# Kernel optimization log

Hardware: AMD Instinct MI355X
Metric: run time of the kernel (lower is better)

## Reference

```python
import jax, jax.numpy as jnp
import numpy as np

O, T, DIN, H, DOUT = 50000, 500000, 128, 256, 128


def setup_inputs() -> dict:
    key = jax.random.key(0)
    ks = jax.random.split(key, 12)
    s = 0.05
    return {
        "obj_vecs": jax.random.normal(ks[0], (O, DIN), jnp.float32),
        "pred_vecs": jax.random.normal(ks[1], (T, DIN), jnp.float32),
        "edges": jax.random.randint(ks[2], (T, 2), 0, O, jnp.int64),
        "w1a": jax.random.normal(ks[3], (3 * DIN, H), jnp.float32) * s,
        "b1a": jax.random.normal(ks[4], (H,), jnp.float32) * s,
        "w1b": jax.random.normal(ks[5], (H, 2 * H + DOUT), jnp.float32) * s,
        "b1b": jax.random.normal(ks[6], (2 * H + DOUT,), jnp.float32) * s,
        "w2a": jax.random.normal(ks[7], (H, H), jnp.float32) * s,
        "b2a": jax.random.normal(ks[8], (H,), jnp.float32) * s,
        "w2b": jax.random.normal(ks[9], (H, DOUT), jnp.float32) * s,
        "b2b": jax.random.normal(ks[10], (DOUT,), jnp.float32) * s,
    }


def reference(obj_vecs, pred_vecs, edges, w1a, b1a, w1b, b1b, w2a, b2a, w2b, b2b):
    n_obj = obj_vecs.shape[0]
    h_dim = w2a.shape[0]
    d_out = w2b.shape[1]
    s_idx = edges[:, 0]
    o_idx = edges[:, 1]
    # gather subject/object node features, concat with predicate: [T, 3*Din]
    cur_t = jnp.concatenate([obj_vecs[s_idx], pred_vecs, obj_vecs[o_idx]], axis=1)
    # edge MLP (net1): Linear-ReLU-Linear-ReLU -> [T, 2H + Dout]
    new_t = jax.nn.relu(jax.nn.relu(cur_t @ w1a + b1a) @ w1b + b1b)
    new_s = new_t[:, :h_dim]
    new_p = new_t[:, h_dim:h_dim + d_out]
    new_o = new_t[:, h_dim + d_out:]
    # scatter-add pooling back to nodes, both endpoints
    idx = jnp.concatenate([s_idx, o_idx])
    vals = jnp.concatenate([new_s, new_o], axis=0)
    pooled = jax.ops.segment_sum(vals, idx, num_segments=n_obj)
    # avg pooling: divide by per-node incidence count (clamped to >= 1)
    counts = jax.ops.segment_sum(jnp.ones(idx.shape[0], obj_vecs.dtype), idx,
                                 num_segments=n_obj)
    pooled = pooled / jnp.clip(counts, 1.0)[:, None]
    # node MLP (net2)
    new_obj = jax.nn.relu(jax.nn.relu(pooled @ w2a + b2a) @ w2b + b2b)
    return new_obj, new_p
```

## Files before the change

kernel.cpp:

```cpp
#include <hip/hip_runtime.h>


using f32x4 = __attribute__((ext_vector_type(4))) float;
using s16x8 = __attribute__((ext_vector_type(8))) short;
typedef unsigned short u16x8 __attribute__((ext_vector_type(8)));

#define VMCNT4  asm volatile("s_waitcnt vmcnt(4)" ::: "memory")
#define VMCNT8  asm volatile("s_waitcnt vmcnt(8)" ::: "memory")
#define VMCNT16 asm volatile("s_waitcnt vmcnt(16)" ::: "memory")
#define VMCNT20 asm volatile("s_waitcnt vmcnt(20)" ::: "memory")
#define VMCNT36 asm volatile("s_waitcnt vmcnt(36)" ::: "memory")
#define LGKM0   asm volatile("s_waitcnt lgkmcnt(0)" ::: "memory")
#define BAR     __builtin_amdgcn_s_barrier()
#define SCHEDB  __builtin_amdgcn_sched_barrier(0)

static __device__ __forceinline__ unsigned short f2b(float f) {
    unsigned int u = __float_as_uint(f);
    unsigned int r = (u + 0x7fffu + ((u >> 16) & 1u)) >> 16;
    return (unsigned short)r;
}

static __device__ __forceinline__ float b2f(unsigned short b) {
    return __uint_as_float(((unsigned)b) << 16);
}

static __device__ __forceinline__ unsigned swz(unsigned row, unsigned byteoff) {
    return byteoff ^ ((row & 7u) << 4);
}

static __device__ __forceinline__ void gload_lds16(const unsigned short* g, unsigned short* l) {
    __builtin_amdgcn_global_load_lds(
        (const __attribute__((address_space(1))) unsigned int*)g,
        (__attribute__((address_space(3))) unsigned int*)l,
        16, 0, 0);
}

__global__ void prep_weights(const float* __restrict__ w1a, const float* __restrict__ w1b,
                             const float* __restrict__ w2a, const float* __restrict__ w2b,
                             unsigned short* __restrict__ w1aT, unsigned short* __restrict__ w1bT,
                             unsigned short* __restrict__ w2aT, unsigned short* __restrict__ w2bT) {
    int t = blockIdx.x * blockDim.x + threadIdx.x;
    if (t < 6 * 16384) {
        int kt = t >> 14;
        int rem = t & 16383; int c = rem >> 6, kk = rem & 63;
        unsigned byte = ((unsigned)(c * 128 + kk * 2)) ^ ((c & 7u) << 4);
        *(unsigned short*)((char*)w1aT + (size_t)kt * 32768 + byte) =
            f2b(w1a[(size_t)(kt * 64 + kk) * 256 + c]);
        return;
    }
    t -= 98304;
    if (t < 10 * 16384) {
        int tile = t >> 14; int nc = tile >> 1, kh = tile & 1;
        int rem = t & 16383; int c = rem >> 7, kk = rem & 127;
        unsigned byte = ((unsigned)(c * 256 + kk * 2)) ^ ((c & 7u) << 4);
        *(unsigned short*)((char*)w1bT + (size_t)tile * 32768 + byte) =
            f2b(w1b[(size_t)(kh * 128 + kk) * 640 + nc * 128 + c]);
        return;
    }
    t -= 163840;
    if (t < 65536) { int n = t >> 8, k = t & 255; w2aT[t] = f2b(w2a[k * 256 + n]); return; }
    t -= 65536;
    if (t < 32768) { int n = t >> 8, k = t & 255; w2bT[t] = f2b(w2b[k * 128 + n]); return; }
}

__global__ void count_slot_kernel(const int* __restrict__ edges, int* __restrict__ cnt,
                                  int* __restrict__ slotS, int* __restrict__ slotO, int T) {
    int e = blockIdx.x * blockDim.x + threadIdx.x;
    if (e < T) {
        slotS[e] = atomicAdd(&cnt[edges[2 * (long long)e]], 1);
        slotO[e] = atomicAdd(&cnt[edges[2 * (long long)e + 1]], 1);
    }
}

__global__ void scan_kernel(const int* __restrict__ cnt, int* __restrict__ rowptr, int O) {
    __shared__ int sc[1024];
    const int tid = threadIdx.x;
    const int per = (O + 1023) >> 10;
    const int base = tid * per;
    int s = 0;
    for (int i = 0; i < per; ++i) { int j = base + i; if (j < O) s += cnt[j]; }
    sc[tid] = s;
    __syncthreads();
    for (int d = 1; d < 1024; d <<= 1) {
        int v = (tid >= d) ? sc[tid - d] : 0;
        __syncthreads();
        sc[tid] += v;
        __syncthreads();
    }
    int off = sc[tid] - s;
    for (int i = 0; i < per; ++i) {
        int j = base + i;
        if (j < O) { rowptr[j] = off; off += cnt[j]; }
    }
    if (tid == 0) rowptr[O] = sc[1023];
}

__global__ void fixup_kernel(const int* __restrict__ edges, const int* __restrict__ rowptr,
                             int* __restrict__ slotS, int* __restrict__ slotO, int T) {
    int e = blockIdx.x * blockDim.x + threadIdx.x;
    if (e < T) {
        slotS[e] += rowptr[edges[2 * (long long)e]];
        slotO[e] += rowptr[edges[2 * (long long)e + 1]];
    }
}

__global__ __launch_bounds__(512, 2) void edge_mlp(
    const float* __restrict__ obj, const float* __restrict__ pred,
    const int* __restrict__ edges,
    const unsigned short* __restrict__ w1aT, const float* __restrict__ b1a,
    const unsigned short* __restrict__ w1bT, const float* __restrict__ b1b,
    const int* __restrict__ slotS, const int* __restrict__ slotO,
    unsigned short* __restrict__ edgeout, float* __restrict__ outP, int T) {
    const int m0 = blockIdx.x * 128;
    const int tid = threadIdx.x;
    const int lane = tid & 63, wid = tid >> 6;
    const int wm = wid >> 2, wn = wid & 3;
    const bool evenL = ((lane & 1) == 0);

    __shared__ unsigned short U[81920];
    char* const ldsb = (char*)U;
    char* const bbase = ldsb + 65536;

    bool okR[4][4];
    #pragma unroll
    for (int mi = 0; mi < 4; ++mi)
        #pragma unroll
        for (int rr = 0; rr < 4; ++rr)
            okR[mi][rr] = (m0 + wm * 64 + mi * 16 + ((lane >> 4) << 2) + rr) < T;

    int slotSr[4][2], slotOr[4][2];
    #pragma unroll
    for (int mi = 0; mi < 4; ++mi)
        #pragma unroll
        for (int k = 0; k < 2; ++k) {
            int rsel = evenL ? k : 2 + k;
            int e = m0 + wm * 64 + mi * 16 + ((lane >> 4) << 2) + rsel;
            if (e >= T) e = T - 1;
            slotSr[mi][k] = slotS[e];
            slotOr[mi][k] = slotO[e];
        }

    const int r = tid >> 2;
    const int q = tid & 3;
    int e_r = m0 + r; if (e_r >= T) e_r = T - 1;
    const int sIdx_r = edges[2 * (long long)e_r];
    const int oIdx_r = edges[2 * (long long)e_r + 1];

    float bias1[4], bias2[5][2];
    #pragma unroll
    for (int nj = 0; nj < 4; ++nj) bias1[nj] = b1a[wn * 64 + nj * 16 + (lane & 15)];
    #pragma unroll
    for (int nc = 0; nc < 5; ++nc)
        #pragma unroll
        for (int nj = 0; nj < 2; ++nj)
            bias2[nc][nj] = b1b[nc * 128 + wn * 32 + nj * 16 + (lane & 15)];

    auto aSrc = [&](int kt) -> const float4* {
        const float* s;
        if (kt < 2)      s = obj  + (long long)sIdx_r * 128 + kt * 64;
        else if (kt < 4) s = pred + (long long)e_r   * 128 + (kt - 2) * 64;
        else             s = obj  + (long long)oIdx_r * 128 + (kt - 4) * 64;
        return (const float4*)s;
    };

    auto tp = [&](int i) -> const unsigned short* {
        return (i < 6) ? (w1aT + (size_t)i * 16384) : (w1bT + (size_t)(i - 6) * 16384);
    };

    auto stage32 = [&](const unsigned short* gt, char* bb) {
        #pragma unroll
        for (int rr4 = 0; rr4 < 4; ++rr4) {
            unsigned off = wid * 4096u + rr4 * 1024u;
            gload_lds16((const unsigned short*)((const char*)gt + off + lane * 16u),
                        (unsigned short*)(bb + off));
        }
    };

    auto writeA = [&](const float4* ap, char* ab) {
        #pragma unroll
        for (int i = 0; i < 4; ++i) {
            float4 v = ap[i];
            ushort4 pk; pk.x = f2b(v.x); pk.y = f2b(v.y); pk.z = f2b(v.z); pk.w = f2b(v.w);
            unsigned byte = (r * 128u + q * 32u + i * 8u) ^ ((r & 7u) << 4);
            *(ushort4*)(ab + byte) = pk;
        }
    };

    f32x4 acc1[4][4];
    #pragma unroll
    for (int a = 0; a < 4; ++a)
        #pragma unroll
        for (int b = 0; b < 4; ++b) acc1[a][b] = f32x4{0.f, 0.f, 0.f, 0.f};

    auto mfma1 = [&](const char* ab, const char* bb) {
        #pragma unroll
        for (int ks = 0; ks < 2; ++ks) {
            const unsigned kk = ks * 32u + ((lane >> 4) << 3);
            s16x8 af[4];
            #pragma unroll
            for (int mi = 0; mi < 4; ++mi) {
                unsigned row = wm * 64u + mi * 16u + (lane & 15);
                af[mi] = *(const s16x8*)(ab + ((row * 128u + kk * 2u) ^ ((row & 7u) << 4)));
            }
            #pragma unroll
            for (int nj = 0; nj < 4; ++nj) {
                unsigned c = wn * 64u + nj * 16u + (lane & 15);
                s16x8 bf = *(const s16x8*)(bb + ((c * 128u + kk * 2u) ^ ((c & 7u) << 4)));
                #pragma unroll
                for (int mi = 0; mi < 4; ++mi)
                    acc1[mi][nj] = __builtin_amdgcn_mfma_f32_16x16x32_bf16(af[mi], bf, acc1[mi][nj], 0, 0, 0);
            }
        }
    };

    float4 ap[4];
    {
        const float4* s4 = aSrc(0);
        #pragma unroll
        for (int i = 0; i < 4; ++i) ap[i] = s4[q * 4 + i];
    }
    writeA(ap, ldsb);
    stage32(tp(0), bbase);
    stage32(tp(1), bbase + 32768);
    {
        const float4* s4 = aSrc(1);
        #pragma unroll
        for (int i = 0; i < 4; ++i) ap[i] = s4[q * 4 + i];
    }
    VMCNT8;
    LGKM0; BAR; SCHEDB;

    #pragma unroll
    for (int s = 0; s < 6; ++s) {
        stage32(tp(s + 2), bbase + ((s + 2) % 3) * 32768);
        __builtin_amdgcn_s_setprio(1);
        mfma1(ldsb + (s & 1) * 16384, bbase + (s % 3) * 32768);
        __builtin_amdgcn_s_setprio(0);
        VMCNT4;
        if (s < 5) {
            writeA(ap, ldsb + ((s + 1) & 1) * 16384);
            if (s < 4) {
                const float4* s4 = aSrc(s + 2);
                #pragma unroll
                for (int i = 0; i < 4; ++i) ap[i] = s4[q * 4 + i];
            }
        }
        LGKM0; BAR; SCHEDB;
    }

    #pragma unroll
    for (int nj = 0; nj < 4; ++nj) {
        unsigned col = wn * 64u + nj * 16u + (lane & 15);
        #pragma unroll
        for (int mi = 0; mi < 4; ++mi)
            #pragma unroll
            for (int rr = 0; rr < 4; ++rr) {
                unsigned row = wm * 64u + mi * 16u + ((lane >> 4) << 2) + rr;
                float v = acc1[mi][nj][rr] + bias1[nj];
                v = v > 0.f ? v : 0.f;
                *(unsigned short*)(ldsb + ((row * 512u + col * 2u) ^ ((row & 7u) << 4))) = f2b(v);
            }
    }
    LGKM0; BAR; SCHEDB;

    #pragma unroll
    for (int nc = 0; nc < 5; ++nc) {
        f32x4 acc2[4][2];
        #pragma unroll
        for (int a = 0; a < 4; ++a)
            #pragma unroll
            for (int b = 0; b < 2; ++b) acc2[a][b] = f32x4{0.f, 0.f, 0.f, 0.f};

        #pragma unroll
        for (int kh = 0; kh < 2; ++kh) {
            const int s = 6 + nc * 2 + kh;
            if (s + 2 <= 15) stage32(tp(s + 2), bbase + ((s + 2) % 3) * 32768);
            const char* bb = bbase + (s % 3) * 32768;
            __builtin_amdgcn_s_setprio(1);
            #pragma unroll
            for (int ks = 0; ks < 4; ++ks) {
                const unsigned kkB = ks * 32u + ((lane >> 4) << 3);
                const unsigned kkH = (kh * 128u) + kkB;
                s16x8 af[4];
                #pragma unroll
                for (int mi = 0; mi < 4; ++mi) {
                    unsigned row = wm * 64u + mi * 16u + (lane & 15);
                    af[mi] = *(const s16x8*)(ldsb + ((row * 512u + kkH * 2u) ^ ((row & 7u) << 4)));
                }
                #pragma unroll
                for (int nj = 0; nj < 2; ++nj) {
                    unsigned c = wn * 32u + nj * 16u + (lane & 15);
                    s16x8 bf = *(const s16x8*)(bb + ((c * 256u + kkB * 2u) ^ ((c & 7u) << 4)));
                    #pragma unroll
                    for (int mi = 0; mi < 4; ++mi)
                        acc2[mi][nj] = __builtin_amdgcn_mfma_f32_16x16x32_bf16(af[mi], bf, acc2[mi][nj], 0, 0, 0);
                }
            }
            __builtin_amdgcn_s_setprio(0);

            if (kh == 0) {
                if (s == 6)       { VMCNT4; }
                else if (s == 12) { VMCNT36; }
                else if (s == 14) { VMCNT16; }
                else              { VMCNT20; }
                LGKM0; BAR; SCHEDB;
            }
        }

        if (nc == 2) {
            #pragma unroll
            for (int nj = 0; nj < 2; ++nj) {
                int col = 2 * 128 + wn * 32 + nj * 16 + (lane & 15);
                #pragma unroll
                for (int mi = 0; mi < 4; ++mi)
                    #pragma unroll
                    for (int rr = 0; rr < 4; ++rr) {
                        int row = wm * 64 + mi * 16 + ((lane >> 4) << 2) + rr;
                        if (okR[mi][rr]) {
                            float v = acc2[mi][nj][rr] + bias2[2][nj];
                            v = v > 0.f ? v : 0.f;
                            outP[(long long)(m0 + row) * 128 + (col - 256)] = v;
                        }
                    }
            }
            VMCNT36;
            LGKM0; BAR; SCHEDB;
        } else {
            #pragma unroll
            for (int nj = 0; nj < 2; ++nj) {
                int col = nc * 128 + wn * 32 + nj * 16 + (lane & 15);
                int pc = (nc < 2) ? col : (col - 384);
                int pcb = (lane & 1) ? (pc - 1) : pc;
                #pragma unroll
                for (int mi = 0; mi < 4; ++mi) {
                    float vv[4];
                    #pragma unroll
                    for (int rr = 0; rr < 4; ++rr) {
                        float v = acc2[mi][nj][rr] + bias2[nc][nj];
                        vv[rr] = v > 0.f ? v : 0.f;
                    }
                    float nb0 = __shfl_xor(vv[0], 1);
                    float nb1 = __shfl_xor(vv[1], 1);
                    float nb2 = __shfl_xor(vv[2], 1);
                    float nb3 = __shfl_xor(vv[3], 1);
                    #pragma unroll
                    for (int k = 0; k < 2; ++k) {
                        float lo = evenL ? (k ? vv[1] : vv[0]) : (k ? nb3 : nb2);
                        float hi = evenL ? (k ? nb1 : nb0) : (k ? vv[3] : vv[2]);
                        int rsel = evenL ? k : 2 + k;
                        if (okR[mi][rsel]) {
                            int slot = (nc < 2) ? slotSr[mi][k] : slotOr[mi][k];
                            unsigned pk = ((unsigned)f2b(hi) << 16) | f2b(lo);
                            *(unsigned*)(edgeout + (size_t)slot * 256 + pcb) = pk;
                        }
                    }
                }
            }
            if (nc < 4) {
                VMCNT20;
                LGKM0; BAR; SCHEDB;
            }
        }
    }
}

__global__ __launch_bounds__(256, 2) void obj_mlp(
    const unsigned short* __restrict__ edgeout, const int* __restrict__ rowptr,
    const unsigned short* __restrict__ w2aT, const float* __restrict__ b2a,
    const unsigned short* __restrict__ w2bT, const float* __restrict__ b2b,
    float* __restrict__ outObj, int O) {
    const int m0 = blockIdx.x * 64;
    const int tid = threadIdx.x;
    const int lane = tid & 63, wid = tid >> 6;
    const int wm = wid >> 1, wn = wid & 1;

    __shared__ unsigned short Abuf[64 * 256];

    for (int it = 0; it < 16; ++it) {
        const int row = it * 4 + wid;
        const int oI = m0 + row;
        float ax = 0.f, ay = 0.f, az = 0.f, aw = 0.f;
        float bx = 0.f, by = 0.f, bz = 0.f, bw = 0.f;
        int n = 0;
        if (oI < O) {
            const int beg = rowptr[oI];
            n = rowptr[oI + 1] - beg;
            const unsigned short* base = edgeout + (size_t)beg * 256 + lane * 4;
            int i = 0;
            for (; i + 3 < n; i += 4) {
                ushort4 v0 = *(const ushort4*)(base + (size_t)(i    ) * 256);
                ushort4 v1 = *(const ushort4*)(base + (size_t)(i + 1) * 256);
                ushort4 v2 = *(const ushort4*)(base + (size_t)(i + 2) * 256);
                ushort4 v3 = *(const ushort4*)(base + (size_t)(i + 3) * 256);
                ax += b2f(v0.x); ay += b2f(v0.y); az += b2f(v0.z); aw += b2f(v0.w);
                bx += b2f(v1.x); by += b2f(v1.y); bz += b2f(v1.z); bw += b2f(v1.w);
                ax += b2f(v2.x); ay += b2f(v2.y); az += b2f(v2.z); aw += b2f(v2.w);
                bx += b2f(v3.x); by += b2f(v3.y); bz += b2f(v3.z); bw += b2f(v3.w);
            }
            for (; i < n; ++i) {
                ushort4 v0 = *(const ushort4*)(base + (size_t)i * 256);
                ax += b2f(v0.x); ay += b2f(v0.y); az += b2f(v0.z); aw += b2f(v0.w);
            }
        }
        float inv = 1.f / fmaxf((float)n, 1.f);
        ushort4 pk;
        pk.x = f2b((ax + bx) * inv); pk.y = f2b((ay + by) * inv);
        pk.z = f2b((az + bz) * inv); pk.w = f2b((aw + bw) * inv);
        unsigned byte = ((unsigned)row * 512u + (unsigned)lane * 8u) ^ (((unsigned)row & 7u) << 4);
        *(ushort4*)((char*)Abuf + byte) = pk;
    }
    __syncthreads();

    f32x4 acc1[2][2][4];
    #pragma unroll
    for (int a = 0; a < 2; ++a)
        #pragma unroll
        for (int b = 0; b < 2; ++b)
            #pragma unroll
            for (int c = 0; c < 4; ++c) acc1[a][b][c] = f32x4{0.f, 0.f, 0.f, 0.f};
    #pragma unroll
    for (int ks = 0; ks < 8; ++ks) {
        const int klane = ks * 32 + ((lane >> 4) << 3);
        s16x8 af[2];
        #pragma unroll
        for (int mi = 0; mi < 2; ++mi) {
            int row = wm * 32 + mi * 16 + (lane & 15);
            af[mi] = *(const s16x8*)((const char*)Abuf + swz(row, row * 512u + klane * 2u));
        }
        #pragma unroll
        for (int nb = 0; nb < 2; ++nb)
            #pragma unroll
            for (int nj = 0; nj < 4; ++nj) {
                int col = nb * 128 + wn * 64 + nj * 16 + (lane & 15);
                s16x8 bf = *(const s16x8*)(w2aT + (long long)col * 256 + klane);
                #pragma unroll
                for (int mi = 0; mi < 2; ++mi)
                    acc1[nb][mi][nj] = __builtin_amdgcn_mfma_f32_16x16x32_bf16(af[mi], bf, acc1[nb][mi][nj], 0, 0, 0);
            }
    }
    __syncthreads();

    #pragma unroll
    for (int nb = 0; nb < 2; ++nb)
        #pragma unroll
        for (int nj = 0; nj < 4; ++nj) {
            int col = nb * 128 + wn * 64 + nj * 16 + (lane & 15);
            float bias = b2a[col];
            #pragma unroll
            for (int mi = 0; mi < 2; ++mi)
                #pragma unroll
                for (int rr = 0; rr < 4; ++rr) {
                    int row = wm * 32 + mi * 16 + ((lane >> 4) << 2) + rr;
                    float v = acc1[nb][mi][nj][rr] + bias;
                    v = v > 0.f ? v : 0.f;
                    *(unsigned short*)((char*)Abuf + swz(row, row * 512u + col * 2u)) = f2b(v);
                }
        }
    __syncthreads();

    f32x4 acc2[2][4];
    #pragma unroll
    for (int b = 0; b < 2; ++b)
        #pragma unroll
        for (int c = 0; c < 4; ++c) acc2[b][c] = f32x4{0.f, 0.f, 0.f, 0.f};
    #pragma unroll
    for (int ks = 0; ks < 8; ++ks) {
        const int klane = ks * 32 + ((lane >> 4) << 3);
        s16x8 af[2];
        #pragma unroll
        for (int mi = 0; mi < 2; ++mi) {
            int row = wm * 32 + mi * 16 + (lane & 15);
            af[mi] = *(const s16x8*)((const char*)Abuf + swz(row, row * 512u + klane * 2u));
        }
        #pragma unroll
        for (int nj = 0; nj < 4; ++nj) {
            int col = wn * 64 + nj * 16 + (lane & 15);
            s16x8 bf = *(const s16x8*)(w2bT + (long long)col * 256 + klane);
            #pragma unroll
            for (int mi = 0; mi < 2; ++mi)
                acc2[mi][nj] = __builtin_amdgcn_mfma_f32_16x16x32_bf16(af[mi], bf, acc2[mi][nj], 0, 0, 0);
        }
    }

    #pragma unroll
    for (int nj = 0; nj < 4; ++nj) {
        int col = wn * 64 + nj * 16 + (lane & 15);
        float bias = b2b[col];
        #pragma unroll
        for (int mi = 0; mi < 2; ++mi)
            #pragma unroll
            for (int rr = 0; rr < 4; ++rr) {
                int row = wm * 32 + mi * 16 + ((lane >> 4) << 2) + rr;
                int o = m0 + row;
                if (o < O) {
                    float v = acc2[mi][nj][rr] + bias;
                    v = v > 0.f ? v : 0.f;
                    outObj[(long long)o * 128 + col] = v;
                }
            }
    }
}

extern "C" void kernel_launch(void* const* d_in, const int* in_sizes, int n_in,
                              void* d_out, int out_size, void* d_ws, size_t ws_size,
                              hipStream_t stream) {
    const float* obj  = (const float*)d_in[0];
    const float* pred = (const float*)d_in[1];
    const int*   edges = (const int*)d_in[2];
    const float* w1a = (const float*)d_in[3];
    const float* b1a = (const float*)d_in[4];
    const float* w1b = (const float*)d_in[5];
    const float* b1b = (const float*)d_in[6];
    const float* w2a = (const float*)d_in[7];
    const float* b2a = (const float*)d_in[8];
    const float* w2b = (const float*)d_in[9];
    const float* b2b = (const float*)d_in[10];

    const int O = in_sizes[0] / 128;
    const int T = in_sizes[1] / 128;

    auto al = [](size_t x) { return (x + 255) & ~(size_t)255; };
    const size_t szEdgeout = (size_t)2 * T * 256 * 2;
    const size_t szCnt     = (size_t)O * 4;
    const size_t szRow     = (size_t)(O + 1) * 4;
    const size_t szSlot    = (size_t)T * 4;

    size_t off = 0;
    char* ws = (char*)d_ws;
    unsigned short* edgeout = (unsigned short*)(ws + off); off += al(szEdgeout);
    int* cnt    = (int*)(ws + off); off += al(szCnt);
    int* rowptr = (int*)(ws + off); off += al(szRow);
    int* slotS  = (int*)(ws + off); off += al(szSlot);
    int* slotO  = (int*)(ws + off); off += al(szSlot);
    unsigned short* w1aT = (unsigned short*)(ws + off); off += (size_t)6 * 16384 * 2;
    unsigned short* w1bT = (unsigned short*)(ws + off); off += (size_t)10 * 16384 * 2;
    unsigned short* w2aT = (unsigned short*)(ws + off); off += (size_t)256 * 256 * 2;
    unsigned short* w2bT = (unsigned short*)(ws + off);

    float* outObj = (float*)d_out;
    float* outP   = (float*)d_out + (size_t)O * 128;

    hipMemsetAsync(cnt, 0, szCnt, stream);
    const int prepElems = 98304 + 163840 + 65536 + 32768;
    prep_weights<<<(prepElems + 255) / 256, 256, 0, stream>>>(w1a, w1b, w2a, w2b, w1aT, w1bT, w2aT, w2bT);
    count_slot_kernel<<<(T + 255) / 256, 256, 0, stream>>>(edges, cnt, slotS, slotO, T);
    scan_kernel<<<1, 1024, 0, stream>>>(cnt, rowptr, O);
    fixup_kernel<<<(T + 255) / 256, 256, 0, stream>>>(edges, rowptr, slotS, slotO, T);
    edge_mlp<<<(T + 127) / 128, 512, 0, stream>>>(obj, pred, edges, w1aT, b1a, w1bT, b1b, slotS, slotO, edgeout, outP, T);
    obj_mlp<<<(O + 63) / 64, 256, 0, stream>>>(edgeout, rowptr, w2aT, b2a, w2bT, b2b, outObj, O);
}
```

Baseline: 901.8 us.

## Merge prep and count kernels, fold slot fixup into edge MLP, tune obj_mlp

Weight preparation and the per-edge count/slot atomics now run in a single launch, and the separate fixup pass is removed by adding rowptr offsets inside edge_mlp when slot indices are loaded. Empty asm statements and a scheduling barrier force those prologue loads to finish before the main pipeline starts. obj_mlp's launch-bounds occupancy hint is raised to 3 and its segment-sum loop is unrolled to 8 edges. These changes cut launch overhead and one full pass over the edge array, at the cost of extra gather loads in the edge_mlp prologue and possible register pressure in obj_mlp.

```diff
diff --git a/kernel.cpp b/kernel.cpp
--- a/kernel.cpp
+++ b/kernel.cpp
@@ -35,11 +35,23 @@
         16, 0, 0);
 }
 
-__global__ void prep_weights(const float* __restrict__ w1a, const float* __restrict__ w1b,
-                             const float* __restrict__ w2a, const float* __restrict__ w2b,
-                             unsigned short* __restrict__ w1aT, unsigned short* __restrict__ w1bT,
-                             unsigned short* __restrict__ w2aT, unsigned short* __restrict__ w2bT) {
+#define PREP_ELEMS (98304 + 163840 + 65536 + 32768)
+
+__global__ void prep_count_kernel(const float* __restrict__ w1a, const float* __restrict__ w1b,
+                                  const float* __restrict__ w2a, const float* __restrict__ w2b,
+                                  unsigned short* __restrict__ w1aT, unsigned short* __restrict__ w1bT,
+                                  unsigned short* __restrict__ w2aT, unsigned short* __restrict__ w2bT,
+                                  const int* __restrict__ edges, int* __restrict__ cnt,
+                                  int* __restrict__ slotS, int* __restrict__ slotO, int T) {
     int t = blockIdx.x * blockDim.x + threadIdx.x;
+    if (t >= PREP_ELEMS) {
+        int e = t - PREP_ELEMS;
+        if (e < T) {
+            slotS[e] = atomicAdd(&cnt[edges[2 * (long long)e]], 1);
+            slotO[e] = atomicAdd(&cnt[edges[2 * (long long)e + 1]], 1);
+        }
+        return;
+    }
     if (t < 6 * 16384) {
         int kt = t >> 14;
         int rem = t & 16383; int c = rem >> 6, kk = rem & 63;
@@ -61,15 +73,6 @@
     if (t < 65536) { int n = t >> 8, k = t & 255; w2aT[t] = f2b(w2a[k * 256 + n]); return; }
     t -= 65536;
     if (t < 32768) { int n = t >> 8, k = t & 255; w2bT[t] = f2b(w2b[k * 128 + n]); return; }
-}
-
-__global__ void count_slot_kernel(const int* __restrict__ edges, int* __restrict__ cnt,
-                                  int* __restrict__ slotS, int* __restrict__ slotO, int T) {
-    int e = blockIdx.x * blockDim.x + threadIdx.x;
-    if (e < T) {
-        slotS[e] = atomicAdd(&cnt[edges[2 * (long long)e]], 1);
-        slotO[e] = atomicAdd(&cnt[edges[2 * (long long)e + 1]], 1);
-    }
 }
 
 __global__ void scan_kernel(const int* __restrict__ cnt, int* __restrict__ rowptr, int O) {
@@ -95,21 +98,13 @@
     if (tid == 0) rowptr[O] = sc[1023];
 }
 
-__global__ void fixup_kernel(const int* __restrict__ edges, const int* __restrict__ rowptr,
-                             int* __restrict__ slotS, int* __restrict__ slotO, int T) {
-    int e = blockIdx.x * blockDim.x + threadIdx.x;
-    if (e < T) {
-        slotS[e] += rowptr[edges[2 * (long long)e]];
-        slotO[e] += rowptr[edges[2 * (long long)e + 1]];
-    }
-}
-
 __global__ __launch_bounds__(512, 2) void edge_mlp(
     const float* __restrict__ obj, const float* __restrict__ pred,
     const int* __restrict__ edges,
     const unsigned short* __restrict__ w1aT, const float* __restrict__ b1a,
     const unsigned short* __restrict__ w1bT, const float* __restrict__ b1b,
     const int* __restrict__ slotS, const int* __restrict__ slotO,
+    const int* __restrict__ rowptr,
     unsigned short* __restrict__ edgeout, float* __restrict__ outP, int T) {
     const int m0 = blockIdx.x * 128;
     const int tid = threadIdx.x;
@@ -136,8 +131,10 @@
             int rsel = evenL ? k : 2 + k;
             int e = m0 + wm * 64 + mi * 16 + ((lane >> 4) << 2) + rsel;
             if (e >= T) e = T - 1;
-            slotSr[mi][k] = slotS[e];
-            slotOr[mi][k] = slotO[e];
+            int si = edges[2 * (long long)e];
+            int oi = edges[2 * (long long)e + 1];
+            slotSr[mi][k] = slotS[e] + rowptr[si];
+            slotOr[mi][k] = slotO[e] + rowptr[oi];
         }
 
     const int r = tid >> 2;
@@ -154,6 +151,20 @@
         #pragma unroll
         for (int nj = 0; nj < 2; ++nj)
             bias2[nc][nj] = b1b[nc * 128 + wn * 32 + nj * 16 + (lane & 15)];
+
+    #pragma unroll
+    for (int mi = 0; mi < 4; ++mi)
+        #pragma unroll
+        for (int k = 0; k < 2; ++k)
+            asm volatile("" :: "v"(slotSr[mi][k]), "v"(slotOr[mi][k]));
+    #pragma unroll
+    for (int nj = 0; nj < 4; ++nj) asm volatile("" :: "v"(bias1[nj]));
+    #pragma unroll
+    for (int nc = 0; nc < 5; ++nc)
+        #pragma unroll
+        for (int nj = 0; nj < 2; ++nj) asm volatile("" :: "v"(bias2[nc][nj]));
+    asm volatile("" :: "v"((float)sIdx_r), "v"((float)oIdx_r));
+    SCHEDB;
 
     auto aSrc = [&](int kt) -> const float4* {
         const float* s;
@@ -364,7 +375,7 @@
     }
 }
 
-__global__ __launch_bounds__(256, 2) void obj_mlp(
+__global__ __launch_bounds__(256, 3) void obj_mlp(
     const unsigned short* __restrict__ edgeout, const int* __restrict__ rowptr,
     const unsigned short* __restrict__ w2aT, const float* __restrict__ b2a,
     const unsigned short* __restrict__ w2bT, const float* __restrict__ b2b,
@@ -387,15 +398,23 @@
             n = rowptr[oI + 1] - beg;
             const unsigned short* base = edgeout + (size_t)beg * 256 + lane * 4;
             int i = 0;
-            for (; i + 3 < n; i += 4) {
+            for (; i + 7 < n; i += 8) {
                 ushort4 v0 = *(const ushort4*)(base + (size_t)(i    ) * 256);
                 ushort4 v1 = *(const ushort4*)(base + (size_t)(i + 1) * 256);
                 ushort4 v2 = *(const ushort4*)(base + (size_t)(i + 2) * 256);
                 ushort4 v3 = *(const ushort4*)(base + (size_t)(i + 3) * 256);
+                ushort4 v4 = *(const ushort4*)(base + (size_t)(i + 4) * 256);
+                ushort4 v5 = *(const ushort4*)(base + (size_t)(i + 5) * 256);
+                ushort4 v6 = *(const ushort4*)(base + (size_t)(i + 6) * 256);
+                ushort4 v7 = *(const ushort4*)(base + (size_t)(i + 7) * 256);
                 ax += b2f(v0.x); ay += b2f(v0.y); az += b2f(v0.z); aw += b2f(v0.w);
                 bx += b2f(v1.x); by += b2f(v1.y); bz += b2f(v1.z); bw += b2f(v1.w);
                 ax += b2f(v2.x); ay += b2f(v2.y); az += b2f(v2.z); aw += b2f(v2.w);
                 bx += b2f(v3.x); by += b2f(v3.y); bz += b2f(v3.z); bw += b2f(v3.w);
+                ax += b2f(v4.x); ay += b2f(v4.y); az += b2f(v4.z); aw += b2f(v4.w);
+                bx += b2f(v5.x); by += b2f(v5.y); bz += b2f(v5.z); bw += b2f(v5.w);
+                ax += b2f(v6.x); ay += b2f(v6.y); az += b2f(v6.z); aw += b2f(v6.w);
+                bx += b2f(v7.x); by += b2f(v7.y); bz += b2f(v7.z); bw += b2f(v7.w);
             }
             for (; i < n; ++i) {
                 ushort4 v0 = *(const ushort4*)(base + (size_t)i * 256);
@@ -541,11 +560,11 @@
     float* outP   = (float*)d_out + (size_t)O * 128;
 
     hipMemsetAsync(cnt, 0, szCnt, stream);
-    const int prepElems = 98304 + 163840 + 65536 + 32768;
-    prep_weights<<<(prepElems + 255) / 256, 256, 0, stream>>>(w1a, w1b, w2a, w2b, w1aT, w1bT, w2aT, w2bT);
-    count_slot_kernel<<<(T + 255) / 256, 256, 0, stream>>>(edges, cnt, slotS, slotO, T);
+    const int totalT = PREP_ELEMS + T;
+    prep_count_kernel<<<(totalT + 255) / 256, 256, 0, stream>>>(
+        w1a, w1b, w2a, w2b, w1aT, w1bT, w2aT, w2bT, edges, cnt, slotS, slotO, T);
     scan_kernel<<<1, 1024, 0, stream>>>(cnt, rowptr, O);
-    fixup_kernel<<<(T + 255) / 256, 256, 0, stream>>>(edges, rowptr, slotS, slotO, T);
-    edge_mlp<<<(T + 127) / 128, 512, 0, stream>>>(obj, pred, edges, w1aT, b1a, w1bT, b1b, slotS, slotO, edgeout, outP, T);
+    edge_mlp<<<(T + 127) / 128, 512, 0, stream>>>(obj, pred, edges, w1aT, b1a, w1bT, b1b,
+                                                  slotS, slotO, rowptr, edgeout, outP, T);
     obj_mlp<<<(O + 63) / 64, 256, 0, stream>>>(edgeout, rowptr, w2aT, b2a, w2bT, b2b, outObj, O);
 }
```

After: 893.7 us. About the same (-0.9%).
